# Kernel optimization log

Hardware: AMD Instinct MI355X
Metric: run time of the kernel (lower is better)

Reference implementation:

```python
import jax, jax.numpy as jnp
import numpy as np

B, F_DIM, C = 256, 512, 100000
M_MARGIN, S_SCALE, K_VP = 0.4, 64.0, 0.7


def l2norm(x, eps):
    n = jnp.linalg.norm(x, axis=-1, keepdims=True)
    return x / jnp.maximum(n, eps)


def setup_inputs() -> dict:
    key = jax.random.key(0)
    k1, k2, k3, k4 = jax.random.split(key, 4)
    inp = jax.random.normal(k1, (B, F_DIM), dtype=jnp.float32)
    # kaiming_normal_(a=1, fan_in, leaky_relu): std = sqrt(2/(1+a^2))/sqrt(fan_in) = 1/sqrt(F)
    weight = jax.random.normal(k2, (C, F_DIM), dtype=jnp.float32) / np.sqrt(F_DIM)
    queue = jax.random.normal(k3, (C, F_DIM), dtype=jnp.float32)
    label = jax.random.randint(k4, (B,), 0, C, dtype=jnp.int32)
    return {"input": inp, "weight": weight, "queue": queue, "label": label, "epoch": 5}


def reference(input, weight, queue, label, epoch):
    emb = l2norm(input, 1e-5)                              # [B, F]
    cos_theta = emb @ l2norm(weight, 1e-5).T               # [B, C]
    one_hot = jax.nn.one_hot(label, C, dtype=cos_theta.dtype)
    cosine = cos_theta - M_MARGIN * one_hot

    # update_virtual_prototype (detached): diag(queue[labels] @ emb.T) == rowwise dot
    emb_d = jax.lax.stop_gradient(emb)
    q_rows = queue[label]                                  # [B, F]
    drift = jnp.sum(q_rows * emb_d, axis=-1)               # [B]
    factor = jax.nn.soft_sign(drift)[:, None]              # softsign update criteria
    new_rows = l2norm(factor * q_rows + (1.0 - factor) * emb_d, 1e-12)
    queue_upd = queue.at[label].set(new_rows)

    # epoch + 1 >= start_vp_epoch (4): virtual-prototype branch
    vp_sim = emb @ jax.lax.stop_gradient(l2norm(queue_upd, 1e-12)).T   # [B, C]
    rows = jnp.arange(B)
    diag = vp_sim[rows, label]
    vp_sim = vp_sim.at[rows, label].set(diag - K_VP * jax.lax.stop_gradient(diag))

    cosine_full = jnp.concatenate([cosine, vp_sim], axis=0)           # [2B, C]
    labels_full = jnp.concatenate([one_hot, one_hot], axis=0)         # [2B, C]
    logits = S_SCALE * cosine_full

    # EPL loss
    sum_neg = jnp.sum((1.0 - labels_full) * jnp.exp(logits), axis=1)
    sum_pos = jnp.sum(labels_full * jnp.exp(-logits), axis=1)
    loss = jnp.log(1.0 + sum_neg * sum_pos)
    return jnp.mean(loss)
```

## Files before the change

kernel.cpp:

```cpp
#include <hip/hip_runtime.h>
#include <math.h>

#define B 256
#define F 512
#define C 100000
#define S_SCALE 64.0f
#define M_MARGIN 0.4f
#define K_VP 0.7f

#define BN 64
#define NTILES ((C + BN - 1) / BN)

typedef __bf16 bf16x8 __attribute__((ext_vector_type(8)));
typedef float  floatx4 __attribute__((ext_vector_type(4)));

__global__ void embnew_kernel(const float* __restrict__ input, const float* __restrict__ queue,
                              const int* __restrict__ label,
                              __bf16* __restrict__ embb_sw, float* __restrict__ newrows) {
    int i = blockIdx.x;
    int t = threadIdx.x;
    const float* x = input + (size_t)i * F;
    float x0 = x[t], x1 = x[t + 256];
    float p = x0 * x0 + x1 * x1;
    __shared__ float red[4];
    for (int off = 32; off > 0; off >>= 1) p += __shfl_down(p, off, 64);
    if ((t & 63) == 0) red[t >> 6] = p;
    __syncthreads();
    float tot = red[0] + red[1] + red[2] + red[3];
    float inv = 1.0f / fmaxf(sqrtf(tot), 1e-5f);
    float e0 = x0 * inv, e1 = x1 * inv;
    {
        int R = i >> 4, ln = i & 15;
        int k = t;
        embb_sw[(size_t)(((R * 16 + (k >> 5)) * 64 + ln + 16 * ((k & 31) >> 3)) * 8 + (k & 7))] = (__bf16)e0;
        k = t + 256;
        embb_sw[(size_t)(((R * 16 + (k >> 5)) * 64 + ln + 16 * ((k & 31) >> 3)) * 8 + (k & 7))] = (__bf16)e1;
    }
    int l = label[i];
    const float* qr = queue + (size_t)l * F;
    float q0 = qr[t], q1 = qr[t + 256];
    float pd = q0 * e0 + q1 * e1;
    __syncthreads();
    for (int off = 32; off > 0; off >>= 1) pd += __shfl_down(pd, off, 64);
    if ((t & 63) == 0) red[t >> 6] = pd;
    __syncthreads();
    float drift = red[0] + red[1] + red[2] + red[3];
    float f = drift / (1.0f + fabsf(drift));
    float v0 = f * q0 + (1.0f - f) * e0;
    float v1 = f * q1 + (1.0f - f) * e1;
    float p2 = v0 * v0 + v1 * v1;
    __syncthreads();
    for (int off = 32; off > 0; off >>= 1) p2 += __shfl_down(p2, off, 64);
    if ((t & 63) == 0) red[t >> 6] = p2;
    __syncthreads();
    float tot2 = red[0] + red[1] + red[2] + red[3];
    float inv2 = 1.0f / fmaxf(sqrtf(tot2), 1e-12f);
    newrows[(size_t)i * F + t]       = v0 * inv2;
    newrows[(size_t)i * F + t + 256] = v1 * inv2;
}

__global__ void init_kernel(int* __restrict__ map) {
    int idx = blockIdx.x * 256 + threadIdx.x;
    if (idx < C) map[idx] = -1;
}

__global__ void scatter_kernel(const int* __restrict__ label, int* __restrict__ map) {
    atomicMax(&map[label[threadIdx.x]], (int)threadIdx.x);
}

__global__ __launch_bounds__(512, 4) void gemm_epl_kernel(
        const __bf16* __restrict__ embb_sw,
        const float* __restrict__ weight,
        const float* __restrict__ queue,
        const float* __restrict__ newrows,
        const int* __restrict__ map,
        const int* __restrict__ label,
        float* __restrict__ partials,
        float* __restrict__ posvals) {
    int bx = blockIdx.x;
    int src = bx / NTILES;
    int tile = bx - src * NTILES;
    int c0 = tile * BN;
    int tid = threadIdx.x;
    int w = tid >> 6;
    int l = tid & 63;
    int ln = l & 15;
    int q = l >> 4;

    __shared__ __align__(16) __bf16 bS[64 * 512];
    __shared__ float colpart_s[BN][9];
    __shared__ float colinv_s[BN];
    __shared__ int label_s[B];

    if (tid < B) label_s[tid] = label[tid];

    {
        int ct = w & 3, h = w >> 2;
        int cl = ct * 16 + ln;
        int c = c0 + cl;
        const float* bp = nullptr;
        if (c < C) {
            if (src == 0) bp = weight + (size_t)c * F;
            else {
                int mi = map[c];
                bp = (mi >= 0) ? newrows + (size_t)mi * F : queue + (size_t)c * F;
            }
        }
        float ss = 0.f;
#pragma unroll
        for (int j2 = 0; j2 < 8; ++j2) {
            int ks = h * 8 + j2;
            int kf = (q + 4 * ks) * 8;
            float4 u0 = make_float4(0.f, 0.f, 0.f, 0.f);
            float4 u1 = make_float4(0.f, 0.f, 0.f, 0.f);
            if (bp) {
                u0 = *(const float4*)(bp + kf);
                u1 = *(const float4*)(bp + kf + 4);
            }
            ss += u0.x * u0.x + u0.y * u0.y + u0.z * u0.z + u0.w * u0.w
                + u1.x * u1.x + u1.y * u1.y + u1.z * u1.z + u1.w * u1.w;
            bf16x8 bv;
            bv[0] = (__bf16)u0.x; bv[1] = (__bf16)u0.y; bv[2] = (__bf16)u0.z; bv[3] = (__bf16)u0.w;
            bv[4] = (__bf16)u1.x; bv[5] = (__bf16)u1.y; bv[6] = (__bf16)u1.z; bv[7] = (__bf16)u1.w;
            *(bf16x8*)&bS[(size_t)(((ks * 4 + ct) * 64 + l) * 8)] = bv;
        }
        colpart_s[cl][h * 4 + q] = ss;
    }
    __syncthreads();

    if (tid < BN) {
        float ssum = 0.f;
#pragma unroll
        for (int p = 0; p < 8; ++p) ssum += colpart_s[tid][p];
        float eps = (src == 0) ? 1e-5f : 1e-12f;
        colinv_s[tid] = 1.0f / fmaxf(sqrtf(ssum), eps);
    }

    floatx4 acc[2][4];
#pragma unroll
    for (int rt = 0; rt < 2; ++rt)
#pragma unroll
        for (int ct = 0; ct < 4; ++ct) acc[rt][ct] = (floatx4){0.f, 0.f, 0.f, 0.f};

    bf16x8 af[2][2];
#pragma unroll
    for (int rt = 0; rt < 2; ++rt)
        af[0][rt] = *(const bf16x8*)(embb_sw + ((size_t)(((w * 2 + rt) * 16 + 0) * 64 + l) << 3));

#pragma unroll
    for (int ks = 0; ks < 16; ++ks) {
        if (ks < 15) {
#pragma unroll
            for (int rt = 0; rt < 2; ++rt)
                af[(ks + 1) & 1][rt] =
                    *(const bf16x8*)(embb_sw + ((size_t)(((w * 2 + rt) * 16 + ks + 1) * 64 + l) << 3));
        }
        bf16x8 bfr[4];
#pragma unroll
        for (int ct = 0; ct < 4; ++ct)
            bfr[ct] = *(const bf16x8*)&bS[(size_t)(((ks * 4 + ct) * 64 + l) * 8)];
#pragma unroll
        for (int rt = 0; rt < 2; ++rt)
#pragma unroll
            for (int ct = 0; ct < 4; ++ct)
                acc[rt][ct] = __builtin_amdgcn_mfma_f32_16x16x32_bf16(af[ks & 1][rt], bfr[ct], acc[rt][ct], 0, 0, 0);
    }

    __syncthreads();

#pragma unroll
    for (int rt = 0; rt < 2; ++rt) {
#pragma unroll
        for (int r = 0; r < 4; ++r) {
            int row = (w * 2 + rt) * 16 + q * 4 + r;
            int lab = label_s[row];
            float sum = 0.f;
#pragma unroll
            for (int ct = 0; ct < 4; ++ct) {
                int c = c0 + ct * 16 + ln;
                if (c < C) {
                    float cosv = acc[rt][ct][r] * colinv_s[ct * 16 + ln];
                    if (c == lab) posvals[src * B + row] = cosv;
                    else sum += __expf(S_SCALE * cosv);
                }
            }
            sum += __shfl_xor(sum, 1, 64);
            sum += __shfl_xor(sum, 2, 64);
            sum += __shfl_xor(sum, 4, 64);
            sum += __shfl_xor(sum, 8, 64);
            if (ln == 0) partials[(size_t)(src * B + row) * NTILES + tile] = sum;
        }
    }
}

__global__ void reduce_kernel(const float* __restrict__ partials, float* __restrict__ negacc) {
    int row = blockIdx.x;
    int t = threadIdx.x;
    float s = 0.f;
    for (int i = t; i < NTILES; i += 256) s += partials[(size_t)row * NTILES + i];
    __shared__ float red[4];
    for (int off = 32; off > 0; off >>= 1) s += __shfl_down(s, off, 64);
    if ((t & 63) == 0) red[t >> 6] = s;
    __syncthreads();
    if (t == 0) negacc[row] = red[0] + red[1] + red[2] + red[3];
}

__global__ void loss_kernel(const float* __restrict__ negacc, const float* __restrict__ posvals,
                            float* __restrict__ out) {
    int t = threadIdx.x;
    float l1 = log1pf(negacc[t] * __expf(-S_SCALE * (posvals[t] - M_MARGIN)));
    float l2 = log1pf(negacc[B + t] * __expf(-S_SCALE * (1.0f - K_VP) * posvals[B + t]));
    float p = l1 + l2;
    __shared__ float red[4];
    for (int off = 32; off > 0; off >>= 1) p += __shfl_down(p, off, 64);
    if ((t & 63) == 0) red[t >> 6] = p;
    __syncthreads();
    if (t == 0) out[0] = (red[0] + red[1] + red[2] + red[3]) / (2.0f * B);
}

extern "C" void kernel_launch(void* const* d_in, const int* in_sizes, int n_in,
                              void* d_out, int out_size, void* d_ws, size_t ws_size,
                              hipStream_t stream) {
    const float* input  = (const float*)d_in[0];
    const float* weight = (const float*)d_in[1];
    const float* queue  = (const float*)d_in[2];
    const int*   label  = (const int*)d_in[3];
    float* out = (float*)d_out;

    char* ws = (char*)d_ws;
    __bf16* embb_sw  = (__bf16*)(ws);
    float*  newrows  = (float*)(ws + (256 << 10));
    float*  negacc   = (float*)(ws + (768 << 10));
    float*  posvals  = (float*)(ws + (768 << 10) + 2048);
    int*    map      = (int*)  (ws + (768 << 10) + 4096);
    float*  partials = (float*)(ws + (1200 << 10));

    init_kernel<<<(C + 255) / 256, 256, 0, stream>>>(map);
    scatter_kernel<<<1, B, 0, stream>>>(label, map);
    embnew_kernel<<<B, 256, 0, stream>>>(input, queue, label, embb_sw, newrows);
    gemm_epl_kernel<<<2 * NTILES, 512, 0, stream>>>(embb_sw, weight, queue, newrows, map,
                                                    label, partials, posvals);
    reduce_kernel<<<2 * B, 256, 0, stream>>>(partials, negacc);
    loss_kernel<<<1, 256, 0, stream>>>(negacc, posvals, out);
}
```

Measured before the change: 478.8 us.

## Make GEMM-EPL kernel persistent with double-buffered LDS and register prefetch

Launches a fixed 256 blocks that each walk a contiguous range of column tiles across both weight and queue sources. The next tile's global loads are issued into registers before the MFMA loop and converted to bf16 afterward, with LDS double-buffered. This targets load latency and per-block setup overhead. It reduces occupancy to fewer resident blocks and relies on software prefetch for memory parallelism. Shared colpart/colinv buffers are reused across iterations with limited synchronization.

Result: slower. 561.1 us (+17.2%).

```diff
diff --git a/kernel.cpp b/kernel.cpp
--- a/kernel.cpp
+++ b/kernel.cpp
@@ -10,6 +10,8 @@
 
 #define BN 64
 #define NTILES ((C + BN - 1) / BN)
+#define NT_TOT (2 * NTILES)
+#define NBLK 256
 
 typedef __bf16 bf16x8 __attribute__((ext_vector_type(8)));
 typedef float  floatx4 __attribute__((ext_vector_type(4)));
@@ -68,7 +70,7 @@
     atomicMax(&map[label[threadIdx.x]], (int)threadIdx.x);
 }
 
-__global__ __launch_bounds__(512, 4) void gemm_epl_kernel(
+__global__ __launch_bounds__(512, 2) void gemm_epl_kernel(
         const __bf16* __restrict__ embb_sw,
         const float* __restrict__ weight,
         const float* __restrict__ queue,
@@ -77,118 +79,148 @@
         const int* __restrict__ label,
         float* __restrict__ partials,
         float* __restrict__ posvals) {
-    int bx = blockIdx.x;
-    int src = bx / NTILES;
-    int tile = bx - src * NTILES;
-    int c0 = tile * BN;
     int tid = threadIdx.x;
     int w = tid >> 6;
     int l = tid & 63;
     int ln = l & 15;
     int q = l >> 4;
-
-    __shared__ __align__(16) __bf16 bS[64 * 512];
+    int ct = w & 3, h = w >> 2;
+    int cl = ct * 16 + ln;
+
+    __shared__ __align__(16) __bf16 bS[2][64 * 512];
     __shared__ float colpart_s[BN][9];
     __shared__ float colinv_s[BN];
     __shared__ int label_s[B];
 
     if (tid < B) label_s[tid] = label[tid];
 
-    {
-        int ct = w & 3, h = w >> 2;
-        int cl = ct * 16 + ln;
-        int c = c0 + cl;
-        const float* bp = nullptr;
-        if (c < C) {
-            if (src == 0) bp = weight + (size_t)c * F;
-            else {
-                int mi = map[c];
-                bp = (mi >= 0) ? newrows + (size_t)mi * F : queue + (size_t)c * F;
+    int ft0 = (int)(((long)blockIdx.x * NT_TOT) / NBLK);
+    int ft1 = (int)(((long)(blockIdx.x + 1) * NT_TOT) / NBLK);
+
+    float4 u[16];
+    bf16x8 sb[8];
+    float ss = 0.f;
+
+    auto colptr = [&](int ft) -> const float* {
+        int s1 = (ft >= NTILES);
+        int tile = ft - s1 * NTILES;
+        int c = tile * BN + cl;
+        if (c >= C) return nullptr;
+        if (!s1) return weight + (size_t)c * F;
+        int mi = map[c];
+        return (mi >= 0) ? newrows + (size_t)mi * F : queue + (size_t)c * F;
+    };
+    auto issue_loads = [&](int ft) {
+        const float* bp = colptr(ft);
+#pragma unroll
+        for (int j2 = 0; j2 < 8; ++j2) {
+            int kf = (q + 4 * (h * 8 + j2)) * 8;
+            if (bp) {
+                u[2 * j2]     = *(const float4*)(bp + kf);
+                u[2 * j2 + 1] = *(const float4*)(bp + kf + 4);
+            } else {
+                u[2 * j2]     = make_float4(0.f, 0.f, 0.f, 0.f);
+                u[2 * j2 + 1] = make_float4(0.f, 0.f, 0.f, 0.f);
             }
         }
-        float ss = 0.f;
+    };
+    auto convert = [&]() {
+        ss = 0.f;
 #pragma unroll
         for (int j2 = 0; j2 < 8; ++j2) {
-            int ks = h * 8 + j2;
-            int kf = (q + 4 * ks) * 8;
-            float4 u0 = make_float4(0.f, 0.f, 0.f, 0.f);
-            float4 u1 = make_float4(0.f, 0.f, 0.f, 0.f);
-            if (bp) {
-                u0 = *(const float4*)(bp + kf);
-                u1 = *(const float4*)(bp + kf + 4);
-            }
+            float4 u0 = u[2 * j2], u1 = u[2 * j2 + 1];
             ss += u0.x * u0.x + u0.y * u0.y + u0.z * u0.z + u0.w * u0.w
                 + u1.x * u1.x + u1.y * u1.y + u1.z * u1.z + u1.w * u1.w;
             bf16x8 bv;
             bv[0] = (__bf16)u0.x; bv[1] = (__bf16)u0.y; bv[2] = (__bf16)u0.z; bv[3] = (__bf16)u0.w;
             bv[4] = (__bf16)u1.x; bv[5] = (__bf16)u1.y; bv[6] = (__bf16)u1.z; bv[7] = (__bf16)u1.w;
-            *(bf16x8*)&bS[(size_t)(((ks * 4 + ct) * 64 + l) * 8)] = bv;
+            sb[j2] = bv;
+        }
+    };
+
+    issue_loads(ft0);
+    convert();
+
+    for (int ft = ft0; ft < ft1; ++ft) {
+        int buf = ft & 1;
+        int s1 = (ft >= NTILES);
+        int tile = ft - s1 * NTILES;
+        int c0 = tile * BN;
+
+#pragma unroll
+        for (int j2 = 0; j2 < 8; ++j2) {
+            int ks = h * 8 + j2;
+            *(bf16x8*)&bS[buf][(((ks * 4 + ct) * 64 + l) * 8)] = sb[j2];
         }
         colpart_s[cl][h * 4 + q] = ss;
-    }
-    __syncthreads();
-
-    if (tid < BN) {
-        float ssum = 0.f;
-#pragma unroll
-        for (int p = 0; p < 8; ++p) ssum += colpart_s[tid][p];
-        float eps = (src == 0) ? 1e-5f : 1e-12f;
-        colinv_s[tid] = 1.0f / fmaxf(sqrtf(ssum), eps);
-    }
-
-    floatx4 acc[2][4];
-#pragma unroll
-    for (int rt = 0; rt < 2; ++rt)
-#pragma unroll
-        for (int ct = 0; ct < 4; ++ct) acc[rt][ct] = (floatx4){0.f, 0.f, 0.f, 0.f};
-
-    bf16x8 af[2][2];
-#pragma unroll
-    for (int rt = 0; rt < 2; ++rt)
-        af[0][rt] = *(const bf16x8*)(embb_sw + ((size_t)(((w * 2 + rt) * 16 + 0) * 64 + l) << 3));
-
-#pragma unroll
-    for (int ks = 0; ks < 16; ++ks) {
-        if (ks < 15) {
+        __syncthreads();
+
+        if (tid < BN) {
+            float ssum = 0.f;
+#pragma unroll
+            for (int p = 0; p < 8; ++p) ssum += colpart_s[tid][p];
+            colinv_s[tid] = 1.0f / fmaxf(sqrtf(ssum), s1 ? 1e-12f : 1e-5f);
+        }
+
+        bool more = (ft + 1 < ft1);
+        if (more) issue_loads(ft + 1);
+
+        floatx4 acc[2][4];
+#pragma unroll
+        for (int rt = 0; rt < 2; ++rt)
+#pragma unroll
+            for (int c2 = 0; c2 < 4; ++c2) acc[rt][c2] = (floatx4){0.f, 0.f, 0.f, 0.f};
+
+        bf16x8 af[2][2];
+#pragma unroll
+        for (int rt = 0; rt < 2; ++rt)
+            af[0][rt] = *(const bf16x8*)(embb_sw + ((size_t)(((w * 2 + rt) * 16 + 0) * 64 + l) << 3));
+
+#pragma unroll
+        for (int ks = 0; ks < 16; ++ks) {
+            if (ks < 15) {
+#pragma unroll
+                for (int rt = 0; rt < 2; ++rt)
+                    af[(ks + 1) & 1][rt] =
+                        *(const bf16x8*)(embb_sw + ((size_t)(((w * 2 + rt) * 16 + ks + 1) * 64 + l) << 3));
+            }
+            bf16x8 bfr[4];
+#pragma unroll
+            for (int c2 = 0; c2 < 4; ++c2)
+                bfr[c2] = *(const bf16x8*)&bS[buf][(((ks * 4 + c2) * 64 + l) * 8)];
 #pragma unroll
             for (int rt = 0; rt < 2; ++rt)
-                af[(ks + 1) & 1][rt] =
-                    *(const bf16x8*)(embb_sw + ((size_t)(((w * 2 + rt) * 16 + ks + 1) * 64 + l) << 3));
-        }
-        bf16x8 bfr[4];
-#pragma unroll
-        for (int ct = 0; ct < 4; ++ct)
-            bfr[ct] = *(const bf16x8*)&bS[(size_t)(((ks * 4 + ct) * 64 + l) * 8)];
-#pragma unroll
-        for (int rt = 0; rt < 2; ++rt)
-#pragma unroll
-            for (int ct = 0; ct < 4; ++ct)
-                acc[rt][ct] = __builtin_amdgcn_mfma_f32_16x16x32_bf16(af[ks & 1][rt], bfr[ct], acc[rt][ct], 0, 0, 0);
-    }
-
-    __syncthreads();
-
-#pragma unroll
-    for (int rt = 0; rt < 2; ++rt) {
-#pragma unroll
-        for (int r = 0; r < 4; ++r) {
-            int row = (w * 2 + rt) * 16 + q * 4 + r;
-            int lab = label_s[row];
-            float sum = 0.f;
-#pragma unroll
-            for (int ct = 0; ct < 4; ++ct) {
-                int c = c0 + ct * 16 + ln;
-                if (c < C) {
-                    float cosv = acc[rt][ct][r] * colinv_s[ct * 16 + ln];
-                    if (c == lab) posvals[src * B + row] = cosv;
-                    else sum += __expf(S_SCALE * cosv);
+#pragma unroll
+                for (int c2 = 0; c2 < 4; ++c2)
+                    acc[rt][c2] = __builtin_amdgcn_mfma_f32_16x16x32_bf16(af[ks & 1][rt], bfr[c2], acc[rt][c2], 0, 0, 0);
+        }
+
+        if (more) convert();
+
+        __syncthreads();
+
+#pragma unroll
+        for (int rt = 0; rt < 2; ++rt) {
+#pragma unroll
+            for (int r = 0; r < 4; ++r) {
+                int row = (w * 2 + rt) * 16 + q * 4 + r;
+                int lab = label_s[row];
+                float sum = 0.f;
+#pragma unroll
+                for (int c2 = 0; c2 < 4; ++c2) {
+                    int c = c0 + c2 * 16 + ln;
+                    if (c < C) {
+                        float cosv = acc[rt][c2][r] * colinv_s[c2 * 16 + ln];
+                        if (c == lab) posvals[s1 * B + row] = cosv;
+                        else sum += __expf(S_SCALE * cosv);
+                    }
                 }
+                sum += __shfl_xor(sum, 1, 64);
+                sum += __shfl_xor(sum, 2, 64);
+                sum += __shfl_xor(sum, 4, 64);
+                sum += __shfl_xor(sum, 8, 64);
+                if (ln == 0) partials[(size_t)(s1 * B + row) * NTILES + tile] = sum;
             }
-            sum += __shfl_xor(sum, 1, 64);
-            sum += __shfl_xor(sum, 2, 64);
-            sum += __shfl_xor(sum, 4, 64);
-            sum += __shfl_xor(sum, 8, 64);
-            if (ln == 0) partials[(size_t)(src * B + row) * NTILES + tile] = sum;
         }
     }
 }
@@ -238,8 +270,8 @@
     init_kernel<<<(C + 255) / 256, 256, 0, stream>>>(map);
     scatter_kernel<<<1, B, 0, stream>>>(label, map);
     embnew_kernel<<<B, 256, 0, stream>>>(input, queue, label, embb_sw, newrows);
-    gemm_epl_kernel<<<2 * NTILES, 512, 0, stream>>>(embb_sw, weight, queue, newrows, map,
-                                                    label, partials, posvals);
+    gemm_epl_kernel<<<NBLK, 512, 0, stream>>>(embb_sw, weight, queue, newrows, map,
+                                              label, partials, posvals);
     reduce_kernel<<<2 * B, 256, 0, stream>>>(partials, negacc);
     loss_kernel<<<1, 256, 0, stream>>>(negacc, posvals, out);
 }
```
